# Kernel tuning notes

Measured on AMD Instinct MI355X. Metric: run time of the kernel, lower is better.

Reference implementation:

```python
import jax, jax.numpy as jnp
import numpy as np
from jax.ops import segment_sum

GRID = 32        # cells per axis; offset grid is (GRID+1)^3
T = 48           # number of accepted MC topologies
N_PTS = 131072

# 12 cube edges: base (lower) corner offset and axis the edge runs along.
# e0..3: x/y edges of z=0 face, e4..7: same at z=1, e8..11: vertical z edges.
EDGE_BASE = np.array([[0,0,0],[1,0,0],[0,1,0],[0,0,0],
                      [0,0,1],[1,0,1],[0,1,1],[0,0,1],
                      [0,0,0],[1,0,0],[1,1,0],[0,1,0]], dtype=np.int32)
EDGE_AXIS = np.array([0,1,0,1, 0,1,0,1, 2,2,2,2], dtype=np.int32)
EDGE_DIR  = np.eye(3, dtype=np.float32)[EDGE_AXIS]          # [12,3] unit dirs


def _dot(u, v):
    return jnp.sum(u * v, axis=-1)


def _safe_div(n, d, eps=1e-12):
    return n / jnp.where(jnp.abs(d) > eps, d, eps)


def _point_tri_dist_sq(p, a, b, c):
    """Squared distance from p to triangle (a,b,c); Ericson closest-point
    algorithm with full vertex/edge/interior region clamping, vectorized.
    p broadcasts against a/b/c over leading dims; last dim is xyz."""
    ab = b - a; ac = c - a; ap = p - a
    d1 = _dot(ab, ap); d2 = _dot(ac, ap)
    bp = p - b; d3 = _dot(ab, bp); d4 = _dot(ac, bp)
    cp = p - c; d5 = _dot(ab, cp); d6 = _dot(ac, cp)
    vc = d1 * d4 - d3 * d2
    vb = d5 * d2 - d1 * d6
    va = d3 * d6 - d5 * d4
    v_ab = _safe_div(d1, d1 - d3)
    w_ac = _safe_div(d2, d2 - d6)
    w_bc = _safe_div(d4 - d3, (d4 - d3) + (d5 - d6))
    inv = _safe_div(jnp.ones_like(va), va + vb + vc)
    v_in = vb * inv; w_in = vc * inv
    q = a + ab * v_in[..., None] + ac * w_in[..., None]                      # interior
    q = jnp.where(((va <= 0) & ((d4 - d3) >= 0) & ((d5 - d6) >= 0))[..., None],
                  b + (c - b) * w_bc[..., None], q)                          # edge BC
    q = jnp.where(((vb <= 0) & (d2 >= 0) & (d6 <= 0))[..., None],
                  a + ac * w_ac[..., None], q)                               # edge AC
    q = jnp.where(((d6 >= 0) & (d5 <= d6))[..., None], c, q)                 # vertex C
    q = jnp.where(((vc <= 0) & (d1 >= 0) & (d3 <= 0))[..., None],
                  a + ab * v_ab[..., None], q)                               # edge AB
    q = jnp.where(((d3 >= 0) & (d4 <= d3))[..., None], b, q)                 # vertex B
    q = jnp.where(((d1 <= 0) & (d2 <= 0))[..., None], a, q)                  # vertex A
    diff = p - q
    return _dot(diff, diff)


def setup_inputs() -> dict:
    key = jax.random.key(0)
    k1, k2, k3 = jax.random.split(key, 3)
    offset = jax.random.uniform(k1, (3, GRID + 1, GRID + 1, GRID + 1), dtype=jnp.float32)
    points = jax.random.uniform(k2, (N_PTS, 3), dtype=jnp.float32) * GRID
    tri_table = jax.random.randint(k3, (T, 3, 3), 0, 12, dtype=jnp.int32)
    return {"offset": offset, "points": points, "tri_table": tri_table}


def reference(offset, points, tri_table):
    edge_base_i = jnp.asarray(EDGE_BASE)                 # [12,3] int
    edge_base_f = jnp.asarray(EDGE_BASE, dtype=offset.dtype)
    edge_dir = jnp.asarray(EDGE_DIR, dtype=offset.dtype)
    edge_axis = jnp.asarray(EDGE_AXIS)

    cell = jnp.clip(jnp.floor(points).astype(jnp.int32), 0, GRID - 1)   # [N,3]
    local = points - cell.astype(points.dtype)                          # [N,3] in [0,1)^3

    # grid index of each edge's base corner -> edge offset parameter t in [0,1]
    gidx = cell[:, None, :] + edge_base_i[None, :, :]                   # [N,12,3]
    t = offset[edge_axis[None, :], gidx[..., 0], gidx[..., 1], gidx[..., 2]]  # [N,12]
    verts = edge_base_f[None] + edge_dir[None] * t[..., None]           # [N,12,3] local coords

    tri = verts[:, tri_table]                                           # [N,T,3tri,3vert,3]
    a = tri[:, :, :, 0, :]; b = tri[:, :, :, 1, :]; c = tri[:, :, :, 2, :]
    p = local[:, None, None, :]                                         # [N,1,1,3]
    d2 = _point_tri_dist_sq(p, a, b, c)                                 # [N,T,3]
    d_min = jnp.min(d2, axis=-1)                                        # [N,T]

    cell_id = (cell[:, 0] * GRID + cell[:, 1]) * GRID + cell[:, 2]      # [N]
    distances_full = segment_sum(d_min, cell_id, num_segments=GRID ** 3)  # [GRID^3, T]
    return distances_full
```

## Files before the change

### kernel.cpp

```cpp
#include <hip/hip_runtime.h>

#define GRID 32
#define NT 48
#define BLK 256
#define SPLIT 16
#define PPB (BLK / SPLIT)
#define NCELLS (GRID * GRID * GRID)
#define CAP 32

#define EDGE_PACK ( (0ULL<<0) | (9ULL<<5) | (2ULL<<10) | (8ULL<<15) | \
                    (4ULL<<20) | (13ULL<<25) | (6ULL<<30) | (12ULL<<35) | \
                    (16ULL<<40) | (17ULL<<45) | (19ULL<<50) | (18ULL<<55) )

__device__ __forceinline__ float tri_dist_gram(float AA, float AB, float AC,
                                               float BB, float BC, float CC) {
    float d1 = AA - AB, d2 = AA - AC;
    float d3 = AB - BB, d4 = AB - BC;
    float d5 = AC - BC, d6 = AC - CC;
    float d43 = BB - BC;
    float d56 = CC - BC;
    float vc = d1 * d4 - d3 * d2;
    float vb = d5 * d2 - d1 * d6;
    float va = d3 * d6 - d5 * d4;

    bool cbc = (va <= 0.f) & (d43 >= 0.f) & (d56 >= 0.f);
    bool cac = (vb <= 0.f) & (d2 >= 0.f) & (d6 <= 0.f);
    bool ccc = (d6 >= 0.f) & (d5 <= d6);
    bool cab = (vc <= 0.f) & (d1 >= 0.f) & (d3 <= 0.f);
    bool cbb = (d3 >= 0.f) & (d4 <= d3);
    bool caa = (d1 <= 0.f) & (d2 <= 0.f);

    float nv = vb, nw = vc, den = va + vb + vc;
    bool mode = false;
    nw = cbc ? d43 : nw;  den = cbc ? d43 + d56 : den;  mode = cbc ? true  : mode;
    nv = cac ? 0.f : nv;  nw = cac ? d2  : nw;  den = cac ? d2 - d6 : den;  mode = cac ? false : mode;
    nw = ccc ? 1.f : nw;  den = ccc ? 1.f : den;  mode = ccc ? true  : mode;
    nv = cab ? d1  : nv;  nw = cab ? 0.f : nw;  den = cab ? d1 - d3 : den;  mode = cab ? false : mode;
    nw = cbb ? 0.f : nw;  den = cbb ? 1.f : den;  mode = cbb ? true  : mode;
    nv = caa ? 0.f : nv;  nw = caa ? 0.f : nw;  den = caa ? 1.f : den;  mode = caa ? false : mode;

    float dd  = (fabsf(den) > 1e-12f) ? den : 1e-12f;
    float inv = __builtin_amdgcn_rcpf(dd);
    float vp = nv * inv;
    float wp = nw * inv;
    float u = mode ? 0.f : 1.f - vp - wp;
    float v = mode ? 1.f - wp : vp;
    float e1 = fmaf(AC, wp, fmaf(AB, v, AA * u));
    float e2 = fmaf(BC, wp, fmaf(BB, v, AB * u));
    float e3 = fmaf(CC, wp, fmaf(BC, v, AC * u));
    return fmaf(wp, e3, fmaf(v, e2, u * e1));
}

__global__ __launch_bounds__(BLK) void eval_kernel(
    const float* __restrict__ offset,
    const float* __restrict__ points,
    const int*   __restrict__ tri_table,
    int*         __restrict__ cnt,
    int*         __restrict__ wlist,
    int*         __restrict__ ovf_cnt,
    int*         __restrict__ ovf,
    float*       __restrict__ dmin,
    int n)
{
    __shared__ float4 v_s[PPB * 13];
    __shared__ float  gram[PPB * 144];
    __shared__ int2   goff[NT * 3];

    const int tid = threadIdx.x;
    const int g   = blockIdx.x * BLK + tid;
    const int pt  = g >> 4;
    const int grp = tid & 15;
    const int pl  = tid >> 4;
    const bool active = (pt < n);

    if (tid < NT * 3) {
        int i = tri_table[tid * 3 + 0];
        int j = tri_table[tid * 3 + 1];
        int k = tri_table[tid * 3 + 2];
        int o0 = (i * 13) | ((i * 12 + j) << 8) | ((i * 12 + k) << 16);
        int o1 = (j * 13) | ((j * 12 + k) << 8) | ((k * 13) << 16);
        goff[tid] = make_int2(o0, o1);
    }

    float4 vi = make_float4(0.f, 0.f, 0.f, 0.f);
    if (active) {
        float px = points[pt * 3 + 0];
        float py = points[pt * 3 + 1];
        float pz = points[pt * 3 + 2];
        int cx = min(max((int)floorf(px), 0), GRID - 1);
        int cy = min(max((int)floorf(py), 0), GRID - 1);
        int cz = min(max((int)floorf(pz), 0), GRID - 1);
        if (grp == 0) {
            int cellid = ((cx * GRID) + cy) * GRID + cz;
            int pos = atomicAdd(&cnt[cellid], 1);
            if (pos < CAP) wlist[cellid * CAP + pos] = pt;
            else { int e = atomicAdd(ovf_cnt, 1); ovf[e] = (cellid << 17) | pt; }
        }
        if (grp < 12) {
            float lx = px - (float)cx;
            float ly = py - (float)cy;
            float lz = pz - (float)cz;
            unsigned nib = (unsigned)(EDGE_PACK >> (5 * grp)) & 31u;
            int gx = cx + (int)(nib & 1u);
            int gy = cy + (int)((nib >> 1) & 1u);
            int gz = cz + (int)((nib >> 2) & 1u);
            int ax = (int)(nib >> 3);
            float t = offset[((ax * 33 + gx) * 33 + gy) * 33 + gz];
            float vx = (ax == 0) ? t : (float)(nib & 1u);
            float vy = (ax == 1) ? t : (float)((nib >> 1) & 1u);
            float vz = (ax == 2) ? t : (float)((nib >> 2) & 1u);
            vi = make_float4(lx - vx, ly - vy, lz - vz, 0.0f);
            v_s[pl * 13 + grp] = vi;
        }
    }
    __syncthreads();
    if (active && grp < 12) {
        float* gp = &gram[pl * 144];
        int j = grp;
#pragma unroll
        for (int d = 0; d < 7; d++) {
            float4 vj = v_s[pl * 13 + j];
            float dv = fmaf(vi.z, vj.z, fmaf(vi.y, vj.y, vi.x * vj.x));
            gp[grp * 12 + j] = dv;
            gp[j * 12 + grp] = dv;
            j = (j == 11) ? 0 : j + 1;
        }
    }
    __syncthreads();
    if (!active) return;

    const float* gp = &gram[pl * 144];
    const int2* gofft = &goff[grp * 9];
    float dm[3];
#pragma unroll
    for (int r = 0; r < 3; r++) {
        float dmn;
#pragma unroll
        for (int k = 0; k < 3; k++) {
            int2 o = gofft[r * 3 + k];
            float AA = gp[o.x & 255];
            float AB = gp[(o.x >> 8) & 255];
            float AC = gp[(unsigned)o.x >> 16];
            float BB = gp[o.y & 255];
            float BC = gp[(o.y >> 8) & 255];
            float CC = gp[(unsigned)o.y >> 16];
            float d = tri_dist_gram(AA, AB, AC, BB, BC, CC);
            dmn = (k == 0) ? d : fminf(dmn, d);
        }
        dm[r] = dmn;
    }
    float* dp = &dmin[pt * NT + grp * 3];
    dp[0] = dm[0]; dp[1] = dm[1]; dp[2] = dm[2];
}

__global__ __launch_bounds__(BLK) void reduce_kernel(
    const int*   __restrict__ cnt,
    const int*   __restrict__ wlist,
    const int*   __restrict__ ovf_cnt,
    const int*   __restrict__ ovf,
    const float* __restrict__ dmin,
    float*       __restrict__ out)
{
    const int tid  = threadIdx.x;
    const int grp  = tid & 15;
    const int pl   = tid >> 4;
    const int cell = blockIdx.x * PPB + pl;

    const int c = min(cnt[cell], CAP);
    const int* wl = &wlist[cell * CAP];
    float s0 = 0.f, s1 = 0.f, s2 = 0.f;
    for (int i = 0; i < c; i++) {
        int pt = wl[i];
        const float* dp = &dmin[pt * NT + grp * 3];
        s0 += dp[0]; s1 += dp[1]; s2 += dp[2];
    }
    const int movf = *ovf_cnt;
    for (int e = 0; e < movf; e++) {
        int v = ovf[e];
        if ((v >> 17) == cell) {
            int pt = v & 0x1FFFF;
            const float* dp = &dmin[pt * NT + grp * 3];
            s0 += dp[0]; s1 += dp[1]; s2 += dp[2];
        }
    }
    float* op = &out[cell * NT + grp * 3];
    op[0] = s0; op[1] = s1; op[2] = s2;
}

__global__ __launch_bounds__(BLK) void ptd_kernel(
    const float* __restrict__ offset,
    const float* __restrict__ points,
    const int*   __restrict__ tri_table,
    float*       __restrict__ out,
    int n)
{
    __shared__ float4 v_s[PPB * 13];
    __shared__ float  gram[PPB * 144];
    __shared__ int2   goff[NT * 3];

    const int tid = threadIdx.x;
    const int g   = blockIdx.x * BLK + tid;
    const int pt  = g >> 4;
    const int grp = tid & 15;
    const int pl  = tid >> 4;
    const bool active = (pt < n);

    if (tid < NT * 3) {
        int i = tri_table[tid * 3 + 0];
        int j = tri_table[tid * 3 + 1];
        int k = tri_table[tid * 3 + 2];
        int o0 = (i * 13) | ((i * 12 + j) << 8) | ((i * 12 + k) << 16);
        int o1 = (j * 13) | ((j * 12 + k) << 8) | ((k * 13) << 16);
        goff[tid] = make_int2(o0, o1);
    }

    float4 vi = make_float4(0.f, 0.f, 0.f, 0.f);
    int cx = 0, cy = 0, cz = 0;
    if (active) {
        float px = points[pt * 3 + 0];
        float py = points[pt * 3 + 1];
        float pz = points[pt * 3 + 2];
        cx = min(max((int)floorf(px), 0), GRID - 1);
        cy = min(max((int)floorf(py), 0), GRID - 1);
        cz = min(max((int)floorf(pz), 0), GRID - 1);
        if (grp < 12) {
            float lx = px - (float)cx;
            float ly = py - (float)cy;
            float lz = pz - (float)cz;
            unsigned nib = (unsigned)(EDGE_PACK >> (5 * grp)) & 31u;
            int gx = cx + (int)(nib & 1u);
            int gy = cy + (int)((nib >> 1) & 1u);
            int gz = cz + (int)((nib >> 2) & 1u);
            int ax = (int)(nib >> 3);
            float t = offset[((ax * 33 + gx) * 33 + gy) * 33 + gz];
            float vx = (ax == 0) ? t : (float)(nib & 1u);
            float vy = (ax == 1) ? t : (float)((nib >> 1) & 1u);
            float vz = (ax == 2) ? t : (float)((nib >> 2) & 1u);
            vi = make_float4(lx - vx, ly - vy, lz - vz, 0.0f);
            v_s[pl * 13 + grp] = vi;
        }
    }
    __syncthreads();
    if (active && grp < 12) {
        float* gp = &gram[pl * 144];
        int j = grp;
#pragma unroll
        for (int d = 0; d < 7; d++) {
            float4 vj = v_s[pl * 13 + j];
            float dv = fmaf(vi.z, vj.z, fmaf(vi.y, vj.y, vi.x * vj.x));
            gp[grp * 12 + j] = dv;
            gp[j * 12 + grp] = dv;
            j = (j == 11) ? 0 : j + 1;
        }
    }
    __syncthreads();
    if (!active) return;

    const float* gp = &gram[pl * 144];
    float* outp = out + ((((cx * GRID) + cy) * GRID + cz) * NT);
    const int2* gofft = &goff[grp * 9];
#pragma unroll
    for (int r = 0; r < 3; r++) {
        float dmn;
#pragma unroll
        for (int k = 0; k < 3; k++) {
            int2 o = gofft[r * 3 + k];
            float AA = gp[o.x & 255];
            float AB = gp[(o.x >> 8) & 255];
            float AC = gp[(unsigned)o.x >> 16];
            float BB = gp[o.y & 255];
            float BC = gp[(o.y >> 8) & 255];
            float CC = gp[(unsigned)o.y >> 16];
            float d = tri_dist_gram(AA, AB, AC, BB, BC, CC);
            dmn = (k == 0) ? d : fminf(dmn, d);
        }
        atomicAdd(&outp[grp * 3 + r], dmn);
    }
}

extern "C" void kernel_launch(void* const* d_in, const int* in_sizes, int n_in,
                              void* d_out, int out_size, void* d_ws, size_t ws_size,
                              hipStream_t stream) {
    const float* offset    = (const float*)d_in[0];
    const float* points    = (const float*)d_in[1];
    const int*   tri_table = (const int*)d_in[2];
    float* out = (float*)d_out;
    int n = in_sizes[1] / 3;

    const size_t CNT_BYTES = (size_t)NCELLS * 4;
    const size_t OVFC_OFF  = CNT_BYTES;
    const size_t WL_OFF    = CNT_BYTES + 128;
    const size_t WL_BYTES  = (size_t)NCELLS * CAP * 4;
    const size_t OVF_OFF   = WL_OFF + WL_BYTES;
    const size_t DMIN_OFF  = OVF_OFF + (size_t)n * 4;
    const size_t WS_NEED   = DMIN_OFF + (size_t)n * NT * 4;

    if (ws_size >= WS_NEED) {
        char* ws = (char*)d_ws;
        int*   cnt     = (int*)(ws);
        int*   ovf_cnt = (int*)(ws + OVFC_OFF);
        int*   wlist   = (int*)(ws + WL_OFF);
        int*   ovf     = (int*)(ws + OVF_OFF);
        float* dmin    = (float*)(ws + DMIN_OFF);
        hipMemsetAsync(ws, 0, WL_OFF, stream);
        long total = (long)n * SPLIT;
        int blocks = (int)((total + BLK - 1) / BLK);
        eval_kernel<<<blocks, BLK, 0, stream>>>(offset, points, tri_table,
                                                cnt, wlist, ovf_cnt, ovf, dmin, n);
        reduce_kernel<<<NCELLS / PPB, BLK, 0, stream>>>(cnt, wlist, ovf_cnt, ovf,
                                                        dmin, out);
    } else {
        hipMemsetAsync(d_out, 0, (size_t)out_size * sizeof(float), stream);
        long total = (long)n * SPLIT;
        int blocks = (int)((total + BLK - 1) / BLK);
        ptd_kernel<<<blocks, BLK, 0, stream>>>(offset, points, tri_table, out, n);
    }
}
```

Measured before the change: 119.9 us.

## Write per-point minima into per-cell slots and simplify triangle region selection

The eval kernel now reserves a per-cell slot (up to 16 per cell) through the atomic counter and writes each point's 48 minima straight into a cell-contiguous buffer, with an overflow buffer for extra points. The reduce kernel then streams contiguous rows instead of gathering through a point list, which removes the indirect, scattered reads of dmin. The triangle distance routine also drops several selects: vertex regions now return the precomputed Gram diagonal directly instead of going through the barycentric path. The slot path needs a much larger workspace (NCELLS*16*48 floats) and falls back to the old path when the workspace is too small.

```diff
diff --git a/kernel.cpp b/kernel.cpp
--- a/kernel.cpp
+++ b/kernel.cpp
@@ -7,6 +7,7 @@
 #define PPB (BLK / SPLIT)
 #define NCELLS (GRID * GRID * GRID)
 #define CAP 32
+#define CAP2 16
 
 #define EDGE_PACK ( (0ULL<<0) | (9ULL<<5) | (2ULL<<10) | (8ULL<<15) | \
                     (4ULL<<20) | (13ULL<<25) | (6ULL<<30) | (12ULL<<35) | \
@@ -31,13 +32,10 @@
     bool caa = (d1 <= 0.f) & (d2 <= 0.f);
 
     float nv = vb, nw = vc, den = va + vb + vc;
-    bool mode = false;
-    nw = cbc ? d43 : nw;  den = cbc ? d43 + d56 : den;  mode = cbc ? true  : mode;
-    nv = cac ? 0.f : nv;  nw = cac ? d2  : nw;  den = cac ? d2 - d6 : den;  mode = cac ? false : mode;
-    nw = ccc ? 1.f : nw;  den = ccc ? 1.f : den;  mode = ccc ? true  : mode;
-    nv = cab ? d1  : nv;  nw = cab ? 0.f : nw;  den = cab ? d1 - d3 : den;  mode = cab ? false : mode;
-    nw = cbb ? 0.f : nw;  den = cbb ? 1.f : den;  mode = cbb ? true  : mode;
-    nv = caa ? 0.f : nv;  nw = caa ? 0.f : nw;  den = caa ? 1.f : den;  mode = caa ? false : mode;
+    nw = cbc ? d43 : nw;  den = cbc ? d43 + d56 : den;
+    nv = cac ? 0.f : nv;  nw = cac ? d2  : nw;  den = cac ? d2 - d6 : den;
+    nv = cab ? d1  : nv;  nw = cab ? 0.f : nw;  den = cab ? d1 - d3 : den;
+    bool mode = cbc & !cac & !cab;
 
     float dd  = (fabsf(den) > 1e-12f) ? den : 1e-12f;
     float inv = __builtin_amdgcn_rcpf(dd);
@@ -48,9 +46,14 @@
     float e1 = fmaf(AC, wp, fmaf(AB, v, AA * u));
     float e2 = fmaf(BC, wp, fmaf(BB, v, AB * u));
     float e3 = fmaf(CC, wp, fmaf(BC, v, AC * u));
-    return fmaf(wp, e3, fmaf(v, e2, u * e1));
-}
-
+    float r  = fmaf(wp, e3, fmaf(v, e2, u * e1));
+    r = (ccc & !cab) ? CC : r;
+    r = cbb ? BB : r;
+    r = caa ? AA : r;
+    return r;
+}
+
+template<bool SLOT>
 __global__ __launch_bounds__(BLK) void eval_kernel(
     const float* __restrict__ offset,
     const float* __restrict__ points,
@@ -60,11 +63,13 @@
     int*         __restrict__ ovf_cnt,
     int*         __restrict__ ovf,
     float*       __restrict__ dmin,
+    float*       __restrict__ dmin_ovf,
     int n)
 {
     __shared__ float4 v_s[PPB * 13];
     __shared__ float  gram[PPB * 144];
     __shared__ int2   goff[NT * 3];
+    __shared__ int    pos_s[PPB];
 
     const int tid = threadIdx.x;
     const int g   = blockIdx.x * BLK + tid;
@@ -93,8 +98,16 @@
         if (grp == 0) {
             int cellid = ((cx * GRID) + cy) * GRID + cz;
             int pos = atomicAdd(&cnt[cellid], 1);
-            if (pos < CAP) wlist[cellid * CAP + pos] = pt;
-            else { int e = atomicAdd(ovf_cnt, 1); ovf[e] = (cellid << 17) | pt; }
+            if (SLOT) {
+                int base;
+                if (pos < CAP2) base = cellid * CAP2 + pos;
+                else { int e = atomicAdd(ovf_cnt, 1); ovf[e] = cellid;
+                       base = 0x40000000 | e; }
+                pos_s[pl] = base;
+            } else {
+                if (pos < CAP) wlist[cellid * CAP + pos] = pt;
+                else { int e = atomicAdd(ovf_cnt, 1); ovf[e] = (cellid << 17) | pt; }
+            }
         }
         if (grp < 12) {
             float lx = px - (float)cx;
@@ -149,8 +162,47 @@
         }
         dm[r] = dmn;
     }
-    float* dp = &dmin[pt * NT + grp * 3];
+    float* dp;
+    if (SLOT) {
+        int base = pos_s[pl];
+        dp = (base & 0x40000000)
+               ? &dmin_ovf[(size_t)(base & 0x3FFFFFFF) * NT + grp * 3]
+               : &dmin[(size_t)base * NT + grp * 3];
+    } else {
+        dp = &dmin[(size_t)pt * NT + grp * 3];
+    }
     dp[0] = dm[0]; dp[1] = dm[1]; dp[2] = dm[2];
+}
+
+__global__ __launch_bounds__(BLK) void reduce_slot_kernel(
+    const int*   __restrict__ cnt,
+    const int*   __restrict__ ovf_cnt,
+    const int*   __restrict__ ovf,
+    const float* __restrict__ dmin,
+    const float* __restrict__ dmin_ovf,
+    float*       __restrict__ out)
+{
+    const int tid  = threadIdx.x;
+    const int grp  = tid & 15;
+    const int pl   = tid >> 4;
+    const int cell = blockIdx.x * PPB + pl;
+
+    const int c = min(cnt[cell], CAP2);
+    const float* bp = &dmin[(size_t)cell * CAP2 * NT + grp * 3];
+    float s0 = 0.f, s1 = 0.f, s2 = 0.f;
+    for (int i = 0; i < c; i++) {
+        s0 += bp[0]; s1 += bp[1]; s2 += bp[2];
+        bp += NT;
+    }
+    const int movf = *ovf_cnt;
+    for (int e = 0; e < movf; e++) {
+        if (ovf[e] == cell) {
+            const float* dp = &dmin_ovf[(size_t)e * NT + grp * 3];
+            s0 += dp[0]; s1 += dp[1]; s2 += dp[2];
+        }
+    }
+    float* op = &out[cell * NT + grp * 3];
+    op[0] = s0; op[1] = s1; op[2] = s2;
 }
 
 __global__ __launch_bounds__(BLK) void reduce_kernel(
@@ -171,7 +223,7 @@
     float s0 = 0.f, s1 = 0.f, s2 = 0.f;
     for (int i = 0; i < c; i++) {
         int pt = wl[i];
-        const float* dp = &dmin[pt * NT + grp * 3];
+        const float* dp = &dmin[(size_t)pt * NT + grp * 3];
         s0 += dp[0]; s1 += dp[1]; s2 += dp[2];
     }
     const int movf = *ovf_cnt;
@@ -179,7 +231,7 @@
         int v = ovf[e];
         if ((v >> 17) == cell) {
             int pt = v & 0x1FFFF;
-            const float* dp = &dmin[pt * NT + grp * 3];
+            const float* dp = &dmin[(size_t)pt * NT + grp * 3];
             s0 += dp[0]; s1 += dp[1]; s2 += dp[2];
         }
     }
@@ -289,30 +341,45 @@
 
     const size_t CNT_BYTES = (size_t)NCELLS * 4;
     const size_t OVFC_OFF  = CNT_BYTES;
-    const size_t WL_OFF    = CNT_BYTES + 128;
-    const size_t WL_BYTES  = (size_t)NCELLS * CAP * 4;
-    const size_t OVF_OFF   = WL_OFF + WL_BYTES;
-    const size_t DMIN_OFF  = OVF_OFF + (size_t)n * 4;
-    const size_t WS_NEED   = DMIN_OFF + (size_t)n * NT * 4;
-
-    if (ws_size >= WS_NEED) {
-        char* ws = (char*)d_ws;
-        int*   cnt     = (int*)(ws);
-        int*   ovf_cnt = (int*)(ws + OVFC_OFF);
-        int*   wlist   = (int*)(ws + WL_OFF);
-        int*   ovf     = (int*)(ws + OVF_OFF);
-        float* dmin    = (float*)(ws + DMIN_OFF);
-        hipMemsetAsync(ws, 0, WL_OFF, stream);
-        long total = (long)n * SPLIT;
-        int blocks = (int)((total + BLK - 1) / BLK);
-        eval_kernel<<<blocks, BLK, 0, stream>>>(offset, points, tri_table,
-                                                cnt, wlist, ovf_cnt, ovf, dmin, n);
-        reduce_kernel<<<NCELLS / PPB, BLK, 0, stream>>>(cnt, wlist, ovf_cnt, ovf,
-                                                        dmin, out);
+    const size_t OVF_OFF   = CNT_BYTES + 128;
+    const size_t TAIL_OFF  = (OVF_OFF + (size_t)n * 4 + 255) & ~(size_t)255;
+
+    const size_t DMIN2_BYTES = (size_t)NCELLS * CAP2 * NT * 4;
+    const size_t DOVF_OFF    = TAIL_OFF + DMIN2_BYTES;
+    const size_t WS_SLOT     = DOVF_OFF + (size_t)n * NT * 4;
+
+    const size_t WL_BYTES = (size_t)NCELLS * CAP * 4;
+    const size_t DMIN_OFF = TAIL_OFF + WL_BYTES;
+    const size_t WS_FB    = DMIN_OFF + (size_t)n * NT * 4;
+
+    char* ws = (char*)d_ws;
+    int* cnt     = (int*)(ws);
+    int* ovf_cnt = (int*)(ws + OVFC_OFF);
+    int* ovf     = (int*)(ws + OVF_OFF);
+
+    long total = (long)n * SPLIT;
+    int blocks = (int)((total + BLK - 1) / BLK);
+
+    if (ws_size >= WS_SLOT) {
+        float* dmin2    = (float*)(ws + TAIL_OFF);
+        float* dmin_ovf = (float*)(ws + DOVF_OFF);
+        hipMemsetAsync(ws, 0, OVF_OFF, stream);
+        eval_kernel<true><<<blocks, BLK, 0, stream>>>(
+            offset, points, tri_table, cnt, nullptr, ovf_cnt, ovf,
+            dmin2, dmin_ovf, n);
+        reduce_slot_kernel<<<NCELLS / PPB, BLK, 0, stream>>>(
+            cnt, ovf_cnt, ovf, dmin2, dmin_ovf, out);
+    } else if (ws_size >= WS_FB) {
+        int*   wlist = (int*)(ws + TAIL_OFF);
+        float* dmin  = (float*)(ws + DMIN_OFF);
+        hipMemsetAsync(ws, 0, OVF_OFF, stream);
+        eval_kernel<false><<<blocks, BLK, 0, stream>>>(
+            offset, points, tri_table, cnt, wlist, ovf_cnt, ovf,
+            dmin, nullptr, n);
+        reduce_kernel<<<NCELLS / PPB, BLK, 0, stream>>>(
+            cnt, wlist, ovf_cnt, ovf, dmin, out);
     } else {
         hipMemsetAsync(d_out, 0, (size_t)out_size * sizeof(float), stream);
-        long total = (long)n * SPLIT;
-        int blocks = (int)((total + BLK - 1) / BLK);
         ptd_kernel<<<blocks, BLK, 0, stream>>>(offset, points, tri_table, out, n);
     }
 }
```

New measurement: 112.5 us. 6.2% less time.
